# Optimization experiments

Measured on AMD Instinct MI355X. Metric: run time of the kernel, lower is better.

Reference implementation:

```python
import jax, jax.numpy as jnp
import numpy as np

DIM = 1024
NUM_EXPERTS = 8
TOP_K = 2
HIDDEN = int(DIM * 1.5)  # 1536, matches expert_dim = int(dim * 1.5)


def setup_inputs() -> dict:
    key = jax.random.key(0)
    k_x, k_r, k_w1, k_w2, k_w3 = jax.random.split(key, 5)
    B, T = 2, 4096
    s_in = 1.0 / np.sqrt(DIM)
    s_h = 1.0 / np.sqrt(HIDDEN)
    return {
        "x": jax.random.normal(k_x, (B, T, DIM), dtype=jnp.float32),
        # router: Linear(dim, num_experts, bias=False) -> stored as [C, E]
        "Wr": jax.random.uniform(k_r, (DIM, NUM_EXPERTS), minval=-s_in, maxval=s_in, dtype=jnp.float32),
        # stacked expert weights: w1/w3 [E, C, H], w2 [E, H, C]
        "W1": jax.random.uniform(k_w1, (NUM_EXPERTS, DIM, HIDDEN), minval=-s_in, maxval=s_in, dtype=jnp.float32),
        "W2": jax.random.uniform(k_w2, (NUM_EXPERTS, HIDDEN, DIM), minval=-s_h, maxval=s_h, dtype=jnp.float32),
        "W3": jax.random.uniform(k_w3, (NUM_EXPERTS, DIM, HIDDEN), minval=-s_in, maxval=s_in, dtype=jnp.float32),
    }


def reference(x, Wr, W1, W2, W3):
    B, T, C = x.shape
    xf = x.reshape(-1, C)  # [N, C]
    gate_logits = xf @ Wr  # [N, E]
    w, idx = jax.lax.top_k(gate_logits, TOP_K)  # [N, K]
    w = jax.nn.softmax(w, axis=-1)
    # dense combine weights: zero for non-selected experts -> [N, E]
    comb = jnp.sum(w[:, :, None] * jax.nn.one_hot(idx, NUM_EXPERTS, dtype=w.dtype), axis=1)
    # SwiGLU for all experts (masked-out experts contribute with weight 0)
    h = jnp.einsum('nc,ech->neh', xf, W1)  # [N, E, H]
    g = jnp.einsum('nc,ech->neh', xf, W3)  # [N, E, H]
    y = jnp.einsum('neh,ehc->nec', jax.nn.silu(h) * g, W2)  # [N, E, C]
    out = jnp.einsum('nec,ne->nc', y, comb)
    return out.reshape(B, T, C)
```

## Files before the change

### kernel.cpp

```cpp
#include <hip/hip_runtime.h>
#include <hip/hip_bf16.h>
#include <math.h>

#define DIM   1024
#define NEXP  8
#define HID   1536
#define NTOK  8192
#define NPOS  16384
#define PADR  128

typedef __attribute__((ext_vector_type(8))) short bf16x8;
typedef __attribute__((ext_vector_type(4))) float floatx4;

__device__ __forceinline__ unsigned short f2bf(float f) {
  unsigned int u = __float_as_uint(f);
  u += 0x7FFFu + ((u >> 16) & 1u);
  return (unsigned short)(u >> 16);
}

__device__ __forceinline__ float bf2f(unsigned short h) {
  return __uint_as_float((unsigned int)h << 16);
}

__device__ __forceinline__ void async_cp16(void* lds, const void* g) {
  __builtin_amdgcn_global_load_lds(
      (const __attribute__((address_space(1))) unsigned int*)g,
      (__attribute__((address_space(3))) unsigned int*)lds, 16, 0, 0);
}

__device__ __forceinline__ int2 cnt_off(const int* __restrict__ hdr, int e) {
  int s = 0, c = 0;
#pragma unroll
  for (int i = 0; i < NEXP; ++i) {
    const int v = hdr[i];
    if (i < e) s += v;
    if (i == e) c = v;
  }
  return make_int2(c, s);
}

__global__ __launch_bounds__(256) void moe_router(
    const float* __restrict__ x, const float* __restrict__ Wr,
    int* __restrict__ meta_e, float* __restrict__ meta_w) {
  const int wave = threadIdx.x >> 6, lane = threadIdx.x & 63;
  const int token = blockIdx.x * 4 + wave;
  const float* xr = x + (size_t)token * DIM;
  float acc[NEXP];
#pragma unroll
  for (int e = 0; e < NEXP; ++e) acc[e] = 0.f;
  for (int i = lane; i < DIM; i += 64) {
    const float xv = xr[i];
    const float* wr = Wr + (size_t)i * NEXP;
#pragma unroll
    for (int e = 0; e < NEXP; ++e) acc[e] += xv * wr[e];
  }
#pragma unroll
  for (int off = 32; off > 0; off >>= 1) {
#pragma unroll
    for (int e = 0; e < NEXP; ++e) acc[e] += __shfl_down(acc[e], off);
  }
  if (lane == 0) {
    int i0 = 0; float v0 = acc[0];
#pragma unroll
    for (int e = 1; e < NEXP; ++e) if (acc[e] > v0) { v0 = acc[e]; i0 = e; }
    int i1 = -1; float v1 = -3.4e38f;
#pragma unroll
    for (int e = 0; e < NEXP; ++e) if (e != i0 && acc[e] > v1) { v1 = acc[e]; i1 = e; }
    const float w0 = 1.f / (1.f + expf(v1 - v0));
    meta_e[token * 2 + 0] = i0;
    meta_e[token * 2 + 1] = i1;
    meta_w[token * 2 + 0] = w0;
    meta_w[token * 2 + 1] = 1.f - w0;
  }
}

__global__ __launch_bounds__(256) void moe_hist(
    const int* __restrict__ meta_e, int* __restrict__ hdr) {
  const int idx = blockIdx.x * 256 + threadIdx.x;
  const int lane = threadIdx.x & 63;
  const int e = meta_e[idx];
#pragma unroll
  for (int ex = 0; ex < NEXP; ++ex) {
    const unsigned long long m = __ballot(e == ex);
    if (m && lane == 0) atomicAdd(&hdr[ex], __popcll(m));
  }
}

__global__ __launch_bounds__(256) void moe_build(
    const int* __restrict__ meta_e, int* __restrict__ hdr,
    int* __restrict__ tok, int* __restrict__ inv) {
  const int idx = blockIdx.x * 256 + threadIdx.x;
  const int lane = threadIdx.x & 63;
  const int token = idx >> 1;
  const int e = meta_e[idx];
  int pos = 0;
#pragma unroll
  for (int ex = 0; ex < NEXP; ++ex) {
    const unsigned long long m = __ballot(e == ex);
    if (m) {
      const int leader = (int)__ffsll((long long)m) - 1;
      int base = 0;
      if (lane == leader) base = atomicAdd(&hdr[16 + ex], __popcll(m));
      base = __shfl(base, leader);
      if (e == ex) {
        const int2 co = cnt_off(hdr, ex);
        pos = co.y + base + (int)__popcll(m & ((1ull << lane) - 1ull));
      }
    }
  }
  tok[pos] = token;
  inv[idx] = pos;
}

__global__ __launch_bounds__(256) void moe_gather(
    const float* __restrict__ x, const int* __restrict__ tok,
    unsigned short* __restrict__ Xg) {
  const int pos = blockIdx.x;
  const int t = tok[pos];
  const float4 v = ((const float4*)(x + (size_t)t * DIM))[threadIdx.x];
  ushort4 o = make_ushort4(f2bf(v.x), f2bf(v.y), f2bf(v.z), f2bf(v.w));
  ((ushort4*)(Xg + (size_t)pos * DIM))[threadIdx.x] = o;
}

__global__ __launch_bounds__(256) void moe_transpose_all(
    const float* __restrict__ W1, const float* __restrict__ W3,
    const float* __restrict__ W2,
    unsigned short* __restrict__ W1t, unsigned short* __restrict__ W3t,
    unsigned short* __restrict__ W2t) {
  __shared__ float tile[64][65];
  const int z = blockIdx.z;
  const int which = z >> 3, e = z & 7;
  const float* src; unsigned short* dst; int R, C;
  if (which == 0)      { src = W1; dst = W1t; R = DIM; C = HID; }
  else if (which == 1) { src = W3; dst = W3t; R = DIM; C = HID; }
  else                 { src = W2; dst = W2t; R = HID; C = DIM; }
  const int nbx = C / 64;
  const int bx = blockIdx.x % nbx, by = blockIdx.x / nbx;
  const float* ein = src + (size_t)e * R * C;
  unsigned short* eout = dst + (size_t)e * R * C;
  const int c0 = bx * 64, r0 = by * 64;
  const int lx = threadIdx.x & 15, ly = threadIdx.x >> 4;
#pragma unroll
  for (int it = 0; it < 4; ++it) {
    const int r = ly + it * 16;
    const float4 v = *(const float4*)&ein[(size_t)(r0 + r) * C + c0 + lx * 4];
    tile[r][lx * 4 + 0] = v.x;
    tile[r][lx * 4 + 1] = v.y;
    tile[r][lx * 4 + 2] = v.z;
    tile[r][lx * 4 + 3] = v.w;
  }
  __syncthreads();
  const int r8 = (threadIdx.x & 7) * 8;
  const int ccb = threadIdx.x >> 3;
#pragma unroll
  for (int it = 0; it < 2; ++it) {
    const int cc = ccb + it * 32;
    unsigned int w0 = (unsigned int)f2bf(tile[r8 + 0][cc]) | ((unsigned int)f2bf(tile[r8 + 1][cc]) << 16);
    unsigned int w1 = (unsigned int)f2bf(tile[r8 + 2][cc]) | ((unsigned int)f2bf(tile[r8 + 3][cc]) << 16);
    unsigned int w2 = (unsigned int)f2bf(tile[r8 + 4][cc]) | ((unsigned int)f2bf(tile[r8 + 5][cc]) << 16);
    unsigned int w3 = (unsigned int)f2bf(tile[r8 + 6][cc]) | ((unsigned int)f2bf(tile[r8 + 7][cc]) << 16);
    uint4 o = make_uint4(w0, w1, w2, w3);
    *(uint4*)&eout[(size_t)(c0 + cc) * R + r0 + r8] = o;
  }
}


__global__ __launch_bounds__(256) void moe_gemm1(
    const unsigned short* __restrict__ Xg,
    const unsigned short* __restrict__ W1t,
    const unsigned short* __restrict__ W3t,
    unsigned short* __restrict__ Hbuf,
    const int* __restrict__ hdr) {
  const int e = blockIdx.y;
  const int NT = HID / 64;
  const int tileRow = blockIdx.x / NT;
  const int tileN = blockIdx.x % NT;
  const int2 co = cnt_off(hdr, e);
  const int cnt = co.x;
  if (tileRow * 128 >= cnt) return;
  const int off = co.y;
  const size_t tileM = (size_t)off + (size_t)tileRow * 128;
  const int n0 = tileN * 64;

  __shared__ unsigned short As[2][128 * 32];
  __shared__ unsigned short B1s[2][64 * 32];
  __shared__ unsigned short B3s[2][64 * 32];

  const int lane = threadIdx.x & 63;
  const int wave = threadIdx.x >> 6;
  const int wm = wave >> 1, wn = wave & 1;
  const int rsub = lane >> 2;
  const int ksw  = (((lane & 3) ^ ((lane >> 3) & 3))) * 8;
  const int kf   = (((lane >> 4) ^ ((lane >> 1) & 3))) * 8;

  const unsigned short* pA0 = Xg + (tileM + (size_t)((wave * 2 + 0) * 16 + rsub)) * DIM + ksw;
  const unsigned short* pA1 = Xg + (tileM + (size_t)((wave * 2 + 1) * 16 + rsub)) * DIM + ksw;
  const unsigned short* pB1 = W1t + ((size_t)e * HID + n0 + wave * 16 + rsub) * DIM + ksw;
  const unsigned short* pB3 = W3t + ((size_t)e * HID + n0 + wave * 16 + rsub) * DIM + ksw;

  floatx4 zero = {0.f, 0.f, 0.f, 0.f};
  floatx4 acc_h[4][2], acc_g[4][2];
#pragma unroll
  for (int i = 0; i < 4; ++i)
#pragma unroll
    for (int j = 0; j < 2; ++j) { acc_h[i][j] = zero; acc_g[i][j] = zero; }

#define G1_STAGE(b, KK) \
    async_cp16(&As[b][(wave * 2 + 0) * 512], pA0 + (KK)); \
    async_cp16(&As[b][(wave * 2 + 1) * 512], pA1 + (KK)); \
    async_cp16(&B1s[b][wave * 512], pB1 + (KK)); \
    async_cp16(&B3s[b][wave * 512], pB3 + (KK));

#define G1_COMP(b) { \
    bf16x8 a[4], b1[2], b3[2]; \
    _Pragma("unroll") \
    for (int i = 0; i < 4; ++i) \
      a[i] = *(const bf16x8*)&As[b][(wm * 64 + i * 16 + (lane & 15)) * 32 + kf]; \
    _Pragma("unroll") \
    for (int j = 0; j < 2; ++j) { \
      b1[j] = *(const bf16x8*)&B1s[b][(wn * 32 + j * 16 + (lane & 15)) * 32 + kf]; \
      b3[j] = *(const bf16x8*)&B3s[b][(wn * 32 + j * 16 + (lane & 15)) * 32 + kf]; \
    } \
    _Pragma("unroll") \
    for (int i = 0; i < 4; ++i) \
      _Pragma("unroll") \
      for (int j = 0; j < 2; ++j) { \
        acc_h[i][j] = __builtin_amdgcn_mfma_f32_16x16x32_bf16(a[i], b1[j], acc_h[i][j], 0, 0, 0); \
        acc_g[i][j] = __builtin_amdgcn_mfma_f32_16x16x32_bf16(a[i], b3[j], acc_g[i][j], 0, 0, 0); \
      } \
  }

  G1_STAGE(0, 0)
  __syncthreads();
  int kk = 0;
#pragma unroll 1
  for (int kt = 0; kt < 15; ++kt) {
    G1_STAGE(1, kk + 32) G1_COMP(0) __syncthreads();
    kk += 64;
    G1_STAGE(0, kk)      G1_COMP(1) __syncthreads();
  }
  G1_STAGE(1, kk + 32) G1_COMP(0) __syncthreads();
  G1_COMP(1)
#undef G1_STAGE
#undef G1_COMP

  const int r0 = (lane >> 4) * 4;
  const int cc = lane & 15;
#pragma unroll
  for (int i = 0; i < 4; ++i)
#pragma unroll
    for (int r = 0; r < 4; ++r) {
      const int lrow = tileRow * 128 + wm * 64 + i * 16 + r0 + r;
      if (lrow < cnt) {
        unsigned short* hrow = Hbuf + (size_t)(off + lrow) * HID + n0 + wn * 32 + cc;
#pragma unroll
        for (int j = 0; j < 2; ++j) {
          const float h = acc_h[i][j][r];
          const float g = acc_g[i][j][r];
          const float s = h / (1.f + expf(-h));
          hrow[j * 16] = f2bf(s * g);
        }
      }
    }
}

__global__ __launch_bounds__(256) void moe_gemm2(
    const unsigned short* __restrict__ Hbuf,
    const unsigned short* __restrict__ W2t,
    const int* __restrict__ hdr,
    unsigned short* __restrict__ Y) {
  const int e = blockIdx.y;
  const int NT = DIM / 128;
  const int tileRow = blockIdx.x / NT;
  const int tileN = blockIdx.x % NT;
  const int2 co = cnt_off(hdr, e);
  const int cnt = co.x;
  if (tileRow * 128 >= cnt) return;
  const int off = co.y;
  const size_t tileM = (size_t)off + (size_t)tileRow * 128;
  const int n0 = tileN * 128;

  __shared__ unsigned short As[2][128 * 32];
  __shared__ unsigned short Bs[2][128 * 32];

  const int lane = threadIdx.x & 63;
  const int wave = threadIdx.x >> 6;
  const int wm = wave >> 1, wn = wave & 1;
  const int rsub = lane >> 2;
  const int ksw  = (((lane & 3) ^ ((lane >> 3) & 3))) * 8;
  const int kf   = (((lane >> 4) ^ ((lane >> 1) & 3))) * 8;

  const unsigned short* qA0 = Hbuf + (tileM + (size_t)((wave * 2 + 0) * 16 + rsub)) * HID + ksw;
  const unsigned short* qA1 = Hbuf + (tileM + (size_t)((wave * 2 + 1) * 16 + rsub)) * HID + ksw;
  const unsigned short* qB0 = W2t + ((size_t)e * DIM + n0 + (wave * 2 + 0) * 16 + rsub) * HID + ksw;
  const unsigned short* qB1 = W2t + ((size_t)e * DIM + n0 + (wave * 2 + 1) * 16 + rsub) * HID + ksw;

  floatx4 zero = {0.f, 0.f, 0.f, 0.f};
  floatx4 acc[4][4];
#pragma unroll
  for (int i = 0; i < 4; ++i)
#pragma unroll
    for (int j = 0; j < 4; ++j) acc[i][j] = zero;

#define G2_STAGE(b, KK) \
    async_cp16(&As[b][(wave * 2 + 0) * 512], qA0 + (KK)); \
    async_cp16(&As[b][(wave * 2 + 1) * 512], qA1 + (KK)); \
    async_cp16(&Bs[b][(wave * 2 + 0) * 512], qB0 + (KK)); \
    async_cp16(&Bs[b][(wave * 2 + 1) * 512], qB1 + (KK));

#define G2_COMP(bb) { \
    bf16x8 a[4], b[4]; \
    _Pragma("unroll") \
    for (int i = 0; i < 4; ++i) \
      a[i] = *(const bf16x8*)&As[bb][(wm * 64 + i * 16 + (lane & 15)) * 32 + kf]; \
    _Pragma("unroll") \
    for (int j = 0; j < 4; ++j) \
      b[j] = *(const bf16x8*)&Bs[bb][(wn * 64 + j * 16 + (lane & 15)) * 32 + kf]; \
    _Pragma("unroll") \
    for (int i = 0; i < 4; ++i) \
      _Pragma("unroll") \
      for (int j = 0; j < 4; ++j) \
        acc[i][j] = __builtin_amdgcn_mfma_f32_16x16x32_bf16(a[i], b[j], acc[i][j], 0, 0, 0); \
  }

  G2_STAGE(0, 0)
  __syncthreads();
  int kk = 0;
#pragma unroll 1
  for (int kt = 0; kt < 23; ++kt) {
    G2_STAGE(1, kk + 32) G2_COMP(0) __syncthreads();
    kk += 64;
    G2_STAGE(0, kk)      G2_COMP(1) __syncthreads();
  }
  G2_STAGE(1, kk + 32) G2_COMP(0) __syncthreads();
  G2_COMP(1)
#undef G2_STAGE
#undef G2_COMP

  const int r0 = (lane >> 4) * 4;
  const int cc = lane & 15;
#pragma unroll
  for (int i = 0; i < 4; ++i)
#pragma unroll
    for (int r = 0; r < 4; ++r) {
      const int lrow = tileRow * 128 + wm * 64 + i * 16 + r0 + r;
      if (lrow < cnt) {
        unsigned short* yrow = Y + (size_t)(off + lrow) * DIM + n0 + wn * 64 + cc;
#pragma unroll
        for (int j = 0; j < 4; ++j)
          yrow[j * 16] = f2bf(acc[i][j][r]);
      }
    }
}

__global__ __launch_bounds__(256) void moe_combine(
    const unsigned short* __restrict__ Y, const int* __restrict__ inv,
    const float* __restrict__ meta_w, float* __restrict__ out) {
  const int t = blockIdx.x;
  const int p0 = inv[t * 2 + 0], p1 = inv[t * 2 + 1];
  const float w0 = meta_w[t * 2 + 0], w1 = meta_w[t * 2 + 1];
  const ushort4 a = ((const ushort4*)(Y + (size_t)p0 * DIM))[threadIdx.x];
  const ushort4 b = ((const ushort4*)(Y + (size_t)p1 * DIM))[threadIdx.x];
  float4 o;
  o.x = w0 * bf2f(a.x) + w1 * bf2f(b.x);
  o.y = w0 * bf2f(a.y) + w1 * bf2f(b.y);
  o.z = w0 * bf2f(a.z) + w1 * bf2f(b.z);
  o.w = w0 * bf2f(a.w) + w1 * bf2f(b.w);
  ((float4*)(out + (size_t)t * DIM))[threadIdx.x] = o;
}

extern "C" void kernel_launch(void* const* d_in, const int* in_sizes, int n_in,
                              void* d_out, int out_size, void* d_ws, size_t ws_size,
                              hipStream_t stream) {
  const float* x  = (const float*)d_in[0];
  const float* Wr = (const float*)d_in[1];
  const float* W1 = (const float*)d_in[2];
  const float* W2 = (const float*)d_in[3];
  const float* W3 = (const float*)d_in[4];
  float* out = (float*)d_out;

  char* p = (char*)d_ws;
  auto carve = [&](size_t bytes) { char* r = p; p += (bytes + 255) & ~(size_t)255; return r; };

  int*            hdr    = (int*)carve(256);
  int*            meta_e = (int*)carve((size_t)NTOK * 2 * sizeof(int));
  float*          meta_w = (float*)carve((size_t)NTOK * 2 * sizeof(float));
  int*            tok    = (int*)carve((size_t)NPOS * sizeof(int));
  int*            inv    = (int*)carve((size_t)NTOK * 2 * sizeof(int));
  unsigned short* Xg     = (unsigned short*)carve((size_t)(NPOS + PADR) * DIM * 2);
  unsigned short* Hbuf   = (unsigned short*)carve((size_t)(NPOS + PADR) * HID * 2);
  unsigned short* W1t    = (unsigned short*)carve((size_t)NEXP * HID * DIM * 2);
  unsigned short* W3t    = (unsigned short*)carve((size_t)NEXP * HID * DIM * 2);
  unsigned short* W2t    = (unsigned short*)carve((size_t)NEXP * DIM * HID * 2);
  unsigned short* Y      = Xg;

  hipMemsetAsync(hdr, 0, 256, stream);

  moe_router<<<NTOK / 4, 256, 0, stream>>>(x, Wr, meta_e, meta_w);
  moe_hist<<<NPOS / 256, 256, 0, stream>>>(meta_e, hdr);
  moe_build<<<NPOS / 256, 256, 0, stream>>>(meta_e, hdr, tok, inv);
  moe_gather<<<NPOS, 256, 0, stream>>>(x, tok, Xg);

  moe_transpose_all<<<dim3(384, 1, 24), dim3(256), 0, stream>>>(W1, W3, W2, W1t, W3t, W2t);

  moe_gemm1<<<dim3(64 * (HID / 64), NEXP), 256, 0, stream>>>(Xg, W1t, W3t, Hbuf, hdr);
  moe_gemm2<<<dim3(64 * (DIM / 128), NEXP), 256, 0, stream>>>(Hbuf, W2t, hdr, Y);
  moe_combine<<<NTOK, 256, 0, stream>>>(Y, inv, meta_w, out);
}
```

Baseline: 592.5 us.

## Deepen async LDS pipeline with fine-grained vmcnt/lgkmcnt waits in expert GEMMs

Restructures the double-buffered K loops of both expert GEMMs so two stages are in flight. Each iteration reads fragments into registers, waits only on LDS reads, issues the next global-to-LDS copy into the freed buffer, then runs the MFMAs. It replaces full __syncthreads with s_waitcnt vmcnt(4)/lgkmcnt(0) plus raw barriers, aiming to hide global load latency behind compute. The hand-placed waitcnt counts assume an exact number of outstanding loads per stage, so they are fragile if the compiler emits extra memory ops.

Measured after the change: 579.4 us. -2.2%, faster.

```diff
diff --git a/kernel.cpp b/kernel.cpp
--- a/kernel.cpp
+++ b/kernel.cpp
@@ -38,6 +38,14 @@
   }
   return make_int2(c, s);
 }
+
+#define FENCE asm volatile("" ::: "memory")
+#define WAIT_LGKM0_BAR do { asm volatile("s_waitcnt lgkmcnt(0)" ::: "memory"); \
+    __builtin_amdgcn_s_barrier(); FENCE; } while (0)
+#define WAIT_VM4_BAR   do { asm volatile("s_waitcnt vmcnt(4)" ::: "memory"); \
+    __builtin_amdgcn_s_barrier(); FENCE; } while (0)
+#define WAIT_VM0_BAR   do { asm volatile("s_waitcnt vmcnt(0)" ::: "memory"); \
+    __builtin_amdgcn_s_barrier(); FENCE; } while (0)
 
 __global__ __launch_bounds__(256) void moe_router(
     const float* __restrict__ x, const float* __restrict__ Wr,
@@ -205,44 +213,69 @@
 #pragma unroll
     for (int j = 0; j < 2; ++j) { acc_h[i][j] = zero; acc_g[i][j] = zero; }
 
-#define G1_STAGE(b, KK) \
-    async_cp16(&As[b][(wave * 2 + 0) * 512], pA0 + (KK)); \
-    async_cp16(&As[b][(wave * 2 + 1) * 512], pA1 + (KK)); \
-    async_cp16(&B1s[b][wave * 512], pB1 + (KK)); \
-    async_cp16(&B3s[b][wave * 512], pB3 + (KK));
-
-#define G1_COMP(b) { \
-    bf16x8 a[4], b1[2], b3[2]; \
+#define G1_STAGE(B, KK) \
+    async_cp16(&As[B][(wave * 2 + 0) * 512], pA0 + (KK)); \
+    async_cp16(&As[B][(wave * 2 + 1) * 512], pA1 + (KK)); \
+    async_cp16(&B1s[B][wave * 512], pB1 + (KK)); \
+    async_cp16(&B3s[B][wave * 512], pB3 + (KK));
+
+#define G1_READ(B) \
     _Pragma("unroll") \
     for (int i = 0; i < 4; ++i) \
-      a[i] = *(const bf16x8*)&As[b][(wm * 64 + i * 16 + (lane & 15)) * 32 + kf]; \
+      a[i] = *(const bf16x8*)&As[B][(wm * 64 + i * 16 + (lane & 15)) * 32 + kf]; \
     _Pragma("unroll") \
     for (int j = 0; j < 2; ++j) { \
-      b1[j] = *(const bf16x8*)&B1s[b][(wn * 32 + j * 16 + (lane & 15)) * 32 + kf]; \
-      b3[j] = *(const bf16x8*)&B3s[b][(wn * 32 + j * 16 + (lane & 15)) * 32 + kf]; \
-    } \
+      b1[j] = *(const bf16x8*)&B1s[B][(wn * 32 + j * 16 + (lane & 15)) * 32 + kf]; \
+      b3[j] = *(const bf16x8*)&B3s[B][(wn * 32 + j * 16 + (lane & 15)) * 32 + kf]; \
+    }
+
+#define G1_MFMA \
     _Pragma("unroll") \
     for (int i = 0; i < 4; ++i) \
       _Pragma("unroll") \
       for (int j = 0; j < 2; ++j) { \
         acc_h[i][j] = __builtin_amdgcn_mfma_f32_16x16x32_bf16(a[i], b1[j], acc_h[i][j], 0, 0, 0); \
         acc_g[i][j] = __builtin_amdgcn_mfma_f32_16x16x32_bf16(a[i], b3[j], acc_g[i][j], 0, 0, 0); \
-      } \
-  }
+      }
 
   G1_STAGE(0, 0)
-  __syncthreads();
-  int kk = 0;
+  G1_STAGE(1, 32)
+  WAIT_VM4_BAR;
+  int kk = 64;
 #pragma unroll 1
   for (int kt = 0; kt < 15; ++kt) {
-    G1_STAGE(1, kk + 32) G1_COMP(0) __syncthreads();
+    {
+      bf16x8 a[4], b1[2], b3[2];
+      G1_READ(0)
+      WAIT_LGKM0_BAR;
+      G1_STAGE(0, kk)
+      G1_MFMA
+    }
+    WAIT_VM4_BAR;
+    {
+      bf16x8 a[4], b1[2], b3[2];
+      G1_READ(1)
+      WAIT_LGKM0_BAR;
+      G1_STAGE(1, kk + 32)
+      G1_MFMA
+    }
+    WAIT_VM4_BAR;
     kk += 64;
-    G1_STAGE(0, kk)      G1_COMP(1) __syncthreads();
-  }
-  G1_STAGE(1, kk + 32) G1_COMP(0) __syncthreads();
-  G1_COMP(1)
+  }
+  {
+    bf16x8 a[4], b1[2], b3[2];
+    G1_READ(0)
+    G1_MFMA
+  }
+  WAIT_VM0_BAR;
+  {
+    bf16x8 a[4], b1[2], b3[2];
+    G1_READ(1)
+    G1_MFMA
+  }
 #undef G1_STAGE
-#undef G1_COMP
+#undef G1_READ
+#undef G1_MFMA
 
   const int r0 = (lane >> 4) * 4;
   const int cc = lane & 15;
@@ -302,40 +335,65 @@
 #pragma unroll
     for (int j = 0; j < 4; ++j) acc[i][j] = zero;
 
-#define G2_STAGE(b, KK) \
-    async_cp16(&As[b][(wave * 2 + 0) * 512], qA0 + (KK)); \
-    async_cp16(&As[b][(wave * 2 + 1) * 512], qA1 + (KK)); \
-    async_cp16(&Bs[b][(wave * 2 + 0) * 512], qB0 + (KK)); \
-    async_cp16(&Bs[b][(wave * 2 + 1) * 512], qB1 + (KK));
-
-#define G2_COMP(bb) { \
-    bf16x8 a[4], b[4]; \
+#define G2_STAGE(B, KK) \
+    async_cp16(&As[B][(wave * 2 + 0) * 512], qA0 + (KK)); \
+    async_cp16(&As[B][(wave * 2 + 1) * 512], qA1 + (KK)); \
+    async_cp16(&Bs[B][(wave * 2 + 0) * 512], qB0 + (KK)); \
+    async_cp16(&Bs[B][(wave * 2 + 1) * 512], qB1 + (KK));
+
+#define G2_READ(B) \
     _Pragma("unroll") \
     for (int i = 0; i < 4; ++i) \
-      a[i] = *(const bf16x8*)&As[bb][(wm * 64 + i * 16 + (lane & 15)) * 32 + kf]; \
+      a[i] = *(const bf16x8*)&As[B][(wm * 64 + i * 16 + (lane & 15)) * 32 + kf]; \
     _Pragma("unroll") \
     for (int j = 0; j < 4; ++j) \
-      b[j] = *(const bf16x8*)&Bs[bb][(wn * 64 + j * 16 + (lane & 15)) * 32 + kf]; \
+      b[j] = *(const bf16x8*)&Bs[B][(wn * 64 + j * 16 + (lane & 15)) * 32 + kf];
+
+#define G2_MFMA \
     _Pragma("unroll") \
     for (int i = 0; i < 4; ++i) \
       _Pragma("unroll") \
       for (int j = 0; j < 4; ++j) \
-        acc[i][j] = __builtin_amdgcn_mfma_f32_16x16x32_bf16(a[i], b[j], acc[i][j], 0, 0, 0); \
-  }
+        acc[i][j] = __builtin_amdgcn_mfma_f32_16x16x32_bf16(a[i], b[j], acc[i][j], 0, 0, 0);
 
   G2_STAGE(0, 0)
-  __syncthreads();
-  int kk = 0;
+  G2_STAGE(1, 32)
+  WAIT_VM4_BAR;
+  int kk = 64;
 #pragma unroll 1
   for (int kt = 0; kt < 23; ++kt) {
-    G2_STAGE(1, kk + 32) G2_COMP(0) __syncthreads();
+    {
+      bf16x8 a[4], b[4];
+      G2_READ(0)
+      WAIT_LGKM0_BAR;
+      G2_STAGE(0, kk)
+      G2_MFMA
+    }
+    WAIT_VM4_BAR;
+    {
+      bf16x8 a[4], b[4];
+      G2_READ(1)
+      WAIT_LGKM0_BAR;
+      G2_STAGE(1, kk + 32)
+      G2_MFMA
+    }
+    WAIT_VM4_BAR;
     kk += 64;
-    G2_STAGE(0, kk)      G2_COMP(1) __syncthreads();
-  }
-  G2_STAGE(1, kk + 32) G2_COMP(0) __syncthreads();
-  G2_COMP(1)
+  }
+  {
+    bf16x8 a[4], b[4];
+    G2_READ(0)
+    G2_MFMA
+  }
+  WAIT_VM0_BAR;
+  {
+    bf16x8 a[4], b[4];
+    G2_READ(1)
+    G2_MFMA
+  }
 #undef G2_STAGE
-#undef G2_COMP
+#undef G2_READ
+#undef G2_MFMA
 
   const int r0 = (lane >> 4) * 4;
   const int cc = lane & 15;
```
